# Performance work log

Measured on AMD Instinct MI355X. Metric: run time of the kernel, lower is better.

The kernel has to match this reference:

```python
import jax, jax.numpy as jnp
import numpy as np

B, T, H = 8, 8192, 512
E, R = 4, 16
SCALE = 0.04  # ~1/sqrt(H), keeps activations/logits in a sane range


def setup_inputs() -> dict:
    key = jax.random.key(0)
    ks = jax.random.split(key, 7)
    return {
        "x": jax.random.normal(ks[0], (B, T, H), jnp.float32),
        "gate_w": jax.random.normal(ks[1], (E, H), jnp.float32) * SCALE,
        "thr_w": jax.random.normal(ks[2], (1, H), jnp.float32) * SCALE,
        "fc1_w": jax.random.normal(ks[3], (E, H, H), jnp.float32) * SCALE,
        "lora_A": jax.random.normal(ks[4], (E, H, R), jnp.float32) * SCALE,
        "lora_B": jax.random.normal(ks[5], (E, R, H), jnp.float32) * SCALE,
        "fc2_w": jax.random.normal(ks[6], (E, H, H), jnp.float32) * SCALE,
    }


def reference(x, gate_w, thr_w, fc1_w, lora_A, lora_B, fc2_w):
    b, t, h = x.shape
    e = gate_w.shape[0]
    xf = x.reshape(-1, h)  # [N, H], N = B*T

    # Threshold-gated routing
    gate_logits = jax.nn.softmax(xf @ gate_w.T, axis=-1)          # [N, E]
    thresholds = jax.nn.sigmoid(xf @ thr_w.T) * (1.0 / e)         # [N, 1]
    adapted = gate_logits - thresholds                            # [N, E]
    selected = (adapted >= 0).astype(xf.dtype)                    # [N, E]
    weights = adapted * selected
    wsum = jnp.sum(weights, axis=-1, keepdims=True)
    wsum = jnp.where(wsum == 0, jnp.ones_like(wsum), wsum)
    weights = weights / wsum                                      # [N, E]

    # Experts: fc2(relu(fc1(x)) @ A @ B). Dense over all experts; the
    # weighted combine with zero weights matches the gather/scatter path.
    hidden = jax.nn.relu(jnp.einsum('ni,ehi->neh', xf, fc1_w))    # [N, E, H]
    lo = jnp.einsum('neh,ehr->ner', hidden, lora_A)               # [N, E, R]
    lo = jnp.einsum('ner,ero->neo', lo, lora_B)                   # [N, E, H]
    expert_out = jnp.einsum('neo,edo->ned', lo, fc2_w)            # [N, E, H]

    out = jnp.einsum('ne,ned->nd', weights, expert_out)           # [N, H]
    return out.reshape(b, t, h)
```

## Files before the change

kernel.cpp:

```cpp
#include <hip/hip_runtime.h>
#include <stdint.h>

#define NTOK 65536
#define HD   512
#define EXP  4
#define RK   16

typedef __attribute__((ext_vector_type(8)))  short short8;
typedef __attribute__((ext_vector_type(4)))  float f32x4;
typedef __attribute__((ext_vector_type(16))) float f32x16;

__device__ __forceinline__ unsigned short f2bf(float f) {
  union { float f; unsigned int u; } c; c.f = f;
  return (unsigned short)((c.u + 0x7fffu + ((c.u >> 16) & 1u)) >> 16);
}

__device__ __forceinline__ void gl_lds16(const void* g, void* l) {
  __builtin_amdgcn_global_load_lds((const __attribute__((address_space(1))) void*)g,
                                   (__attribute__((address_space(3))) void*)l, 16, 0, 0);
}

__global__ void convgate(const float* __restrict__ x, const float* __restrict__ gw,
                         const float* __restrict__ tw, unsigned short* __restrict__ xbo,
                         float* __restrict__ gates) {
  const int lane = threadIdx.x & 63;
  const int n = blockIdx.x * 4 + (threadIdx.x >> 6);
  const float4* xr = (const float4*)(x + (size_t)n * HD);
  const float4 xa = xr[lane * 2], xb = xr[lane * 2 + 1];
  ushort4 ua, ub;
  ua.x = f2bf(xa.x); ua.y = f2bf(xa.y); ua.z = f2bf(xa.z); ua.w = f2bf(xa.w);
  ub.x = f2bf(xb.x); ub.y = f2bf(xb.y); ub.z = f2bf(xb.z); ub.w = f2bf(xb.w);
  ushort4* xo = (ushort4*)(xbo + (size_t)n * HD);
  xo[lane * 2] = ua; xo[lane * 2 + 1] = ub;
  float s[5];
#pragma unroll
  for (int e = 0; e < 4; e++) {
    const float4* wr = (const float4*)(gw + e * HD);
    const float4 wa = wr[lane * 2], wb = wr[lane * 2 + 1];
    s[e] = xa.x * wa.x + xa.y * wa.y + xa.z * wa.z + xa.w * wa.w
         + xb.x * wb.x + xb.y * wb.y + xb.z * wb.z + xb.w * wb.w;
  }
  {
    const float4* wr = (const float4*)tw;
    const float4 wa = wr[lane * 2], wb = wr[lane * 2 + 1];
    s[4] = xa.x * wa.x + xa.y * wa.y + xa.z * wa.z + xa.w * wa.w
         + xb.x * wb.x + xb.y * wb.y + xb.z * wb.z + xb.w * wb.w;
  }
#pragma unroll
  for (int off = 32; off > 0; off >>= 1)
#pragma unroll
    for (int i = 0; i < 5; i++) s[i] += __shfl_xor(s[i], off, 64);
  float m = fmaxf(fmaxf(s[0], s[1]), fmaxf(s[2], s[3]));
  float e0 = expf(s[0] - m), e1 = expf(s[1] - m), e2 = expf(s[2] - m), e3 = expf(s[3] - m);
  float inv = 1.f / (e0 + e1 + e2 + e3);
  float thr = 0.25f / (1.f + expf(-s[4]));
  float a0 = e0 * inv - thr, a1 = e1 * inv - thr, a2 = e2 * inv - thr, a3 = e3 * inv - thr;
  float w0 = a0 > 0.f ? a0 : 0.f, w1 = a1 > 0.f ? a1 : 0.f;
  float w2 = a2 > 0.f ? a2 : 0.f, w3 = a3 > 0.f ? a3 : 0.f;
  float wsum = w0 + w1 + w2 + w3;
  wsum = (wsum == 0.f) ? 1.f : wsum;
  if (lane < 4) {
    float wv = lane == 0 ? w0 : lane == 1 ? w1 : lane == 2 ? w2 : w3;
    gates[(size_t)n * 4 + lane] = wv / wsum;
  }
}

__global__ void convk(const float* __restrict__ in, unsigned short* __restrict__ o, int n4) {
  int i = blockIdx.x * 256 + threadIdx.x;
  if (i < n4) {
    float4 v = ((const float4*)in)[i];
    ushort4 u;
    u.x = f2bf(v.x); u.y = f2bf(v.y); u.z = f2bf(v.z); u.w = f2bf(v.w);
    ((ushort4*)o)[i] = u;
  }
}

__global__ void prep_mt(const float* __restrict__ loraB, const float* __restrict__ fc2,
                        unsigned short* __restrict__ Mt) {
  int idx = blockIdx.x * 256 + threadIdx.x;
  int d  = idx & (HD - 1);
  int er = idx >> 9;
  int e = er >> 4, r = er & 15;
  const float4* B = (const float4*)(loraB + ((size_t)e * RK + r) * HD);
  const float4* F = (const float4*)(fc2 + ((size_t)e * HD + d) * HD);
  float a0 = 0.f, a1 = 0.f, a2 = 0.f, a3 = 0.f;
  for (int i = 0; i < HD / 4; i += 4) {
    float4 b0 = B[i],     f0 = F[i];
    float4 b1 = B[i + 1], f1 = F[i + 1];
    float4 b2 = B[i + 2], f2 = F[i + 2];
    float4 b3 = B[i + 3], f3 = F[i + 3];
    a0 += b0.x * f0.x + b0.y * f0.y + b0.z * f0.z + b0.w * f0.w;
    a1 += b1.x * f1.x + b1.y * f1.y + b1.z * f1.z + b1.w * f1.w;
    a2 += b2.x * f2.x + b2.y * f2.y + b2.z * f2.z + b2.w * f2.w;
    a3 += b3.x * f3.x + b3.y * f3.y + b3.z * f3.z + b3.w * f3.w;
  }
  Mt[d * 64 + er] = f2bf(a0 + a1 + a2 + a3);
}

__launch_bounds__(512, 2)
__global__ void fc1_lora(const unsigned short* __restrict__ xb,
                         const unsigned short* __restrict__ w1b,
                         const float* __restrict__ loraA,
                         float* __restrict__ lw) {
  __shared__ __align__(16) char smem[135168];
  const int bid = blockIdx.x;
  const int c = bid & 7;
  const int j = bid >> 3;
  const int eh = j & 7;
  const int e = eh >> 1, hq = eh & 1;
  const int ntile = c * 32 + (j >> 3);
  const int n0 = ntile * 256;
  const int tid = threadIdx.x;
  const int wave = tid >> 6, lane = tid & 63;
  const int l16 = lane & 15, quad = lane >> 4;
  const int l32 = lane & 31, half = lane >> 5;
  const int wr = wave >> 2, wc = wave & 3;

  const unsigned short* xg = xb + (size_t)n0 * HD;
  const unsigned short* wg = w1b + ((size_t)e * HD + (size_t)hq * 256) * HD;

  const unsigned short* xsrc[2];
  const unsigned short* wsrc[2];
#pragma unroll
  for (int i = 0; i < 2; i++) {
    const int sl = tid + 512 * i;
    const int sr = sl >> 3, g8 = (sl & 7) ^ (sr & 7);
    const int row = sr * 2 + (g8 >> 2), g = g8 & 3;
    xsrc[i] = xg + (size_t)row * HD + g * 8;
    wsrc[i] = wg + (size_t)row * HD + g * 8;
  }
  const int wbase = wave * 1024;

  int axo[2][4], bxo[2][2];
#pragma unroll
  for (int kk = 0; kk < 2; kk++) {
#pragma unroll
    for (int mb = 0; mb < 4; mb++) {
      const int rowa = wr * 128 + mb * 32 + l32;
      const int sr = rowa >> 1, g8 = (rowa & 1) * 4 + kk * 2 + half;
      axo[kk][mb] = (sr * 8 + (g8 ^ (sr & 7))) * 16;
    }
#pragma unroll
    for (int nb = 0; nb < 2; nb++) {
      const int rowb = wc * 64 + nb * 32 + l32;
      const int sr = rowb >> 1, g8 = (rowb & 1) * 4 + kk * 2 + half;
      bxo[kk][nb] = (sr * 8 + (g8 ^ (sr & 7))) * 16;
    }
  }

  f32x16 acc[4][2];
#pragma unroll
  for (int mb = 0; mb < 4; mb++)
#pragma unroll
    for (int nb = 0; nb < 2; nb++)
#pragma unroll
      for (int r = 0; r < 16; r++) acc[mb][nb][r] = 0.f;

#pragma unroll
  for (int tt = 0; tt < 3; tt++) {
    char* As = smem + tt * 32768;
#pragma unroll
    for (int i = 0; i < 2; i++) gl_lds16(xsrc[i] + tt * 32, As + wbase + 8192 * i);
#pragma unroll
    for (int i = 0; i < 2; i++) gl_lds16(wsrc[i] + tt * 32, As + 16384 + wbase + 8192 * i);
  }
  asm volatile("s_waitcnt vmcnt(8)\n\ts_barrier" ::: "memory");
  __builtin_amdgcn_sched_barrier(0);

#pragma unroll
  for (int t = 0; t < 16; t++) {
    char* Ab = smem + (t & 3) * 32768;
    char* Bb = Ab + 16384;
    char* As = smem + ((t + 3) & 3) * 32768;
    const int kos = (t + 3) * 32;
#pragma unroll
    for (int p = 0; p < 2; p++) {
      short8 af[4], bf[2];
#pragma unroll
      for (int mb = 0; mb < 4; mb++) af[mb] = *(const short8*)(Ab + axo[p][mb]);
#pragma unroll
      for (int nb = 0; nb < 2; nb++) bf[nb] = *(const short8*)(Bb + bxo[p][nb]);
      if (t < 13) {
        gl_lds16(xsrc[p] + kos, As + wbase + 8192 * p);
        gl_lds16(wsrc[p] + kos, As + 16384 + wbase + 8192 * p);
      }
      asm volatile("s_barrier" ::: "memory");
      __builtin_amdgcn_s_setprio(1);
#pragma unroll
      for (int mb = 0; mb < 4; mb++)
#pragma unroll
        for (int nb = 0; nb < 2; nb++)
          acc[mb][nb] = __builtin_amdgcn_mfma_f32_32x32x16_bf16(af[mb], bf[nb], acc[mb][nb], 0, 0, 0);
      __builtin_amdgcn_s_setprio(0);
    }
    if (t < 13) {
      asm volatile("s_waitcnt lgkmcnt(0)\n\ts_waitcnt vmcnt(8)\n\ts_barrier" ::: "memory");
    } else if (t == 13) {
      asm volatile("s_waitcnt lgkmcnt(0)\n\ts_waitcnt vmcnt(4)\n\ts_barrier" ::: "memory");
    } else if (t == 14) {
      asm volatile("s_waitcnt lgkmcnt(0)\n\ts_waitcnt vmcnt(0)\n\ts_barrier" ::: "memory");
    } else {
      asm volatile("s_waitcnt lgkmcnt(0)\n\ts_barrier" ::: "memory");
    }
    __builtin_amdgcn_sched_barrier(0);
  }

  unsigned short* hsm = (unsigned short*)smem;
#pragma unroll
  for (int mb = 0; mb < 4; mb++)
#pragma unroll
    for (int nb = 0; nb < 2; nb++) {
      const int colh = wc * 64 + nb * 32 + l32;
#pragma unroll
      for (int r = 0; r < 16; r++) {
        const int tok = wr * 128 + mb * 32 + 4 * half + (r & 3) + 8 * (r >> 2);
        float v = acc[mb][nb][r];
        v = v > 0.f ? v : 0.f;
        hsm[tok * 264 + colh] = f2bf(v);
      }
    }
  __syncthreads();

  const float* Ae = loraA + (size_t)e * HD * RK;
  const int hA0 = hq * 256;
  f32x4 lo[2];
#pragma unroll
  for (int mf = 0; mf < 2; mf++)
#pragma unroll
    for (int i = 0; i < 4; i++) lo[mf][i] = 0.f;
#pragma unroll
  for (int k2 = 0; k2 < 8; k2++) {
    short8 a2[2];
#pragma unroll
    for (int mf = 0; mf < 2; mf++) {
      const int tok = wave * 32 + mf * 16 + l16;
      a2[mf] = *(const short8*)(hsm + tok * 264 + k2 * 32 + quad * 8);
    }
    union { short8 v; unsigned short sv[8]; } b2;
#pragma unroll
    for (int j2 = 0; j2 < 8; j2++)
      b2.sv[j2] = f2bf(Ae[(size_t)(hA0 + k2 * 32 + quad * 8 + j2) * RK + l16]);
#pragma unroll
    for (int mf = 0; mf < 2; mf++)
      lo[mf] = __builtin_amdgcn_mfma_f32_16x16x32_bf16(a2[mf], b2.v, lo[mf], 0, 0, 0);
  }
#pragma unroll
  for (int mf = 0; mf < 2; mf++)
#pragma unroll
    for (int i = 0; i < 4; i++)
      atomicAdd(lw + (size_t)(n0 + wave * 32 + mf * 16 + quad * 4 + i) * 64 + e * 16 + l16, lo[mf][i]);
}

__launch_bounds__(256, 2)
__global__ void combine_k(const float* __restrict__ lw, const float* __restrict__ gates,
                          const unsigned short* __restrict__ Mt, float* __restrict__ out) {
  __shared__ __align__(16) char smem[65536];
  const int n0 = blockIdx.x * 64;
  const int tid = threadIdx.x;
  const int wave = tid >> 6, lane = tid & 63, quad = lane >> 4, l16 = lane & 15;
#pragma unroll
  for (int i = 0; i < 16; i++) {
    const int slot = tid + 256 * i;
    const int row = slot >> 3;
    const int g = (slot & 7) ^ (row & 7);
    *(uint4*)(smem + slot * 16) = *(const uint4*)(Mt + row * 64 + g * 8);
  }
  __syncthreads();
  f32x4 acc[4][8];
#pragma unroll
  for (int a = 0; a < 4; a++)
#pragma unroll
    for (int b = 0; b < 8; b++)
#pragma unroll
      for (int i = 0; i < 4; i++) acc[a][b][i] = 0.f;
#pragma unroll
  for (int ks = 0; ks < 2; ks++) {
    short8 af[4], bfr[8];
#pragma unroll
    for (int mf = 0; mf < 4; mf++) {
      const int n = n0 + mf * 16 + l16;
      const float* lr = lw + (size_t)n * 64 + ks * 32 + quad * 8;
      float4 u0 = *(const float4*)lr;
      float4 u1 = *(const float4*)(lr + 4);
      const float g = gates[(size_t)n * 4 + ((ks * 32 + quad * 8) >> 4)];
      union { short8 v; unsigned short s[8]; } a;
      a.s[0] = f2bf(u0.x * g); a.s[1] = f2bf(u0.y * g);
      a.s[2] = f2bf(u0.z * g); a.s[3] = f2bf(u0.w * g);
      a.s[4] = f2bf(u1.x * g); a.s[5] = f2bf(u1.y * g);
      a.s[6] = f2bf(u1.z * g); a.s[7] = f2bf(u1.w * g);
      af[mf] = a.v;
    }
#pragma unroll
    for (int nf = 0; nf < 8; nf++) {
      const int row = wave * 128 + nf * 16 + l16;
      const int slot = row * 8 + ((ks * 4 + quad) ^ (row & 7));
      bfr[nf] = *(const short8*)(smem + slot * 16);
    }
#pragma unroll
    for (int mf = 0; mf < 4; mf++)
#pragma unroll
      for (int nf = 0; nf < 8; nf++)
        acc[mf][nf] = __builtin_amdgcn_mfma_f32_16x16x32_bf16(af[mf], bfr[nf], acc[mf][nf], 0, 0, 0);
  }
#pragma unroll
  for (int mf = 0; mf < 4; mf++)
#pragma unroll
    for (int nf = 0; nf < 8; nf++) {
      const int d = wave * 128 + nf * 16 + l16;
#pragma unroll
      for (int i = 0; i < 4; i++)
        out[(size_t)(n0 + mf * 16 + quad * 4 + i) * HD + d] = acc[mf][nf][i];
    }
}

extern "C" void kernel_launch(void* const* d_in, const int* in_sizes, int n_in,
                              void* d_out, int out_size, void* d_ws, size_t ws_size,
                              hipStream_t stream) {
  const float* x      = (const float*)d_in[0];
  const float* gate_w = (const float*)d_in[1];
  const float* thr_w  = (const float*)d_in[2];
  const float* fc1_w  = (const float*)d_in[3];
  const float* lora_A = (const float*)d_in[4];
  const float* lora_B = (const float*)d_in[5];
  const float* fc2_w  = (const float*)d_in[6];
  float* out = (float*)d_out;
  char* ws = (char*)d_ws;

  unsigned short* xbp = (unsigned short*)(ws);
  unsigned short* w1b = (unsigned short*)(ws + 67108864);
  unsigned short* Mt  = (unsigned short*)(ws + 69206016);
  float*          gts = (float*)(ws + 69271552);
  float*          lwp = (float*)(ws + 70320128);

  hipMemsetAsync(lwp, 0, (size_t)NTOK * 64 * sizeof(float), stream);
  convgate<<<NTOK / 4, 256, 0, stream>>>(x, gate_w, thr_w, xbp, gts);
  convk<<<1024, 256, 0, stream>>>(fc1_w, w1b, EXP * HD * HD / 4);
  prep_mt<<<128, 256, 0, stream>>>(lora_B, fc2_w, Mt);
  fc1_lora<<<2048, 512, 0, stream>>>(xbp, w1b, lora_A, lwp);
  combine_k<<<NTOK / 64, 256, 0, stream>>>(lwp, gts, Mt, out);
}
```

Baseline: 440.7 us.

## Parallelize prep_mt per wave, pre-transpose lora_A, coalesce combine stores, retune barriers

Result: no change. 441.4 us (+0.2%).

```diff
diff --git a/kernel.cpp b/kernel.cpp
--- a/kernel.cpp
+++ b/kernel.cpp
@@ -77,30 +77,34 @@
 
 __global__ void prep_mt(const float* __restrict__ loraB, const float* __restrict__ fc2,
                         unsigned short* __restrict__ Mt) {
+  const int wid = blockIdx.x * 4 + (threadIdx.x >> 6);
+  const int lane = threadIdx.x & 63;
+  const int d = wid & (HD - 1);
+  const int er = wid >> 9;
+  const int e = er >> 4, r = er & 15;
+  const float4* B = (const float4*)(loraB + ((size_t)e * RK + r) * HD);
+  const float4* F = (const float4*)(fc2 + ((size_t)e * HD + d) * HD);
+  const float4 b0 = B[lane * 2], b1 = B[lane * 2 + 1];
+  const float4 f0 = F[lane * 2], f1 = F[lane * 2 + 1];
+  float s = b0.x * f0.x + b0.y * f0.y + b0.z * f0.z + b0.w * f0.w
+          + b1.x * f1.x + b1.y * f1.y + b1.z * f1.z + b1.w * f1.w;
+#pragma unroll
+  for (int off = 32; off > 0; off >>= 1) s += __shfl_xor(s, off, 64);
+  if (lane == 0) Mt[d * 64 + er] = f2bf(s);
+}
+
+__global__ void prep_la(const float* __restrict__ la, unsigned short* __restrict__ laT) {
   int idx = blockIdx.x * 256 + threadIdx.x;
-  int d  = idx & (HD - 1);
+  int h = idx & (HD - 1);
   int er = idx >> 9;
   int e = er >> 4, r = er & 15;
-  const float4* B = (const float4*)(loraB + ((size_t)e * RK + r) * HD);
-  const float4* F = (const float4*)(fc2 + ((size_t)e * HD + d) * HD);
-  float a0 = 0.f, a1 = 0.f, a2 = 0.f, a3 = 0.f;
-  for (int i = 0; i < HD / 4; i += 4) {
-    float4 b0 = B[i],     f0 = F[i];
-    float4 b1 = B[i + 1], f1 = F[i + 1];
-    float4 b2 = B[i + 2], f2 = F[i + 2];
-    float4 b3 = B[i + 3], f3 = F[i + 3];
-    a0 += b0.x * f0.x + b0.y * f0.y + b0.z * f0.z + b0.w * f0.w;
-    a1 += b1.x * f1.x + b1.y * f1.y + b1.z * f1.z + b1.w * f1.w;
-    a2 += b2.x * f2.x + b2.y * f2.y + b2.z * f2.z + b2.w * f2.w;
-    a3 += b3.x * f3.x + b3.y * f3.y + b3.z * f3.z + b3.w * f3.w;
-  }
-  Mt[d * 64 + er] = f2bf(a0 + a1 + a2 + a3);
+  laT[(size_t)er * HD + h] = f2bf(la[((size_t)e * HD + h) * RK + r]);
 }
 
 __launch_bounds__(512, 2)
 __global__ void fc1_lora(const unsigned short* __restrict__ xb,
                          const unsigned short* __restrict__ w1b,
-                         const float* __restrict__ loraA,
+                         const unsigned short* __restrict__ laT,
                          float* __restrict__ lw) {
   __shared__ __align__(16) char smem[135168];
   const int bid = blockIdx.x;
@@ -133,18 +137,18 @@
 
   int axo[2][4], bxo[2][2];
 #pragma unroll
-  for (int kk = 0; kk < 2; kk++) {
+  for (int p = 0; p < 2; p++) {
 #pragma unroll
     for (int mb = 0; mb < 4; mb++) {
       const int rowa = wr * 128 + mb * 32 + l32;
-      const int sr = rowa >> 1, g8 = (rowa & 1) * 4 + kk * 2 + half;
-      axo[kk][mb] = (sr * 8 + (g8 ^ (sr & 7))) * 16;
+      const int sr = rowa >> 1, g8 = (rowa & 1) * 4 + p * 2 + half;
+      axo[p][mb] = (sr * 8 + (g8 ^ (sr & 7))) * 16;
     }
 #pragma unroll
     for (int nb = 0; nb < 2; nb++) {
       const int rowb = wc * 64 + nb * 32 + l32;
-      const int sr = rowb >> 1, g8 = (rowb & 1) * 4 + kk * 2 + half;
-      bxo[kk][nb] = (sr * 8 + (g8 ^ (sr & 7))) * 16;
+      const int sr = rowb >> 1, g8 = (rowb & 1) * 4 + p * 2 + half;
+      bxo[p][nb] = (sr * 8 + (g8 ^ (sr & 7))) * 16;
     }
   }
 
@@ -164,7 +168,8 @@
 #pragma unroll
     for (int i = 0; i < 2; i++) gl_lds16(wsrc[i] + tt * 32, As + 16384 + wbase + 8192 * i);
   }
-  asm volatile("s_waitcnt vmcnt(8)\n\ts_barrier" ::: "memory");
+  asm volatile("s_waitcnt vmcnt(8)" ::: "memory");
+  __builtin_amdgcn_s_barrier();
   __builtin_amdgcn_sched_barrier(0);
 
 #pragma unroll
@@ -184,7 +189,9 @@
         gl_lds16(xsrc[p] + kos, As + wbase + 8192 * p);
         gl_lds16(wsrc[p] + kos, As + 16384 + wbase + 8192 * p);
       }
-      asm volatile("s_barrier" ::: "memory");
+      __builtin_amdgcn_s_barrier();
+      asm volatile("s_waitcnt lgkmcnt(0)" ::: "memory");
+      __builtin_amdgcn_sched_barrier(0);
       __builtin_amdgcn_s_setprio(1);
 #pragma unroll
       for (int mb = 0; mb < 4; mb++)
@@ -192,17 +199,16 @@
         for (int nb = 0; nb < 2; nb++)
           acc[mb][nb] = __builtin_amdgcn_mfma_f32_32x32x16_bf16(af[mb], bf[nb], acc[mb][nb], 0, 0, 0);
       __builtin_amdgcn_s_setprio(0);
-    }
-    if (t < 13) {
-      asm volatile("s_waitcnt lgkmcnt(0)\n\ts_waitcnt vmcnt(8)\n\ts_barrier" ::: "memory");
-    } else if (t == 13) {
-      asm volatile("s_waitcnt lgkmcnt(0)\n\ts_waitcnt vmcnt(4)\n\ts_barrier" ::: "memory");
-    } else if (t == 14) {
-      asm volatile("s_waitcnt lgkmcnt(0)\n\ts_waitcnt vmcnt(0)\n\ts_barrier" ::: "memory");
-    } else {
-      asm volatile("s_waitcnt lgkmcnt(0)\n\ts_barrier" ::: "memory");
-    }
-    __builtin_amdgcn_sched_barrier(0);
+      if (p == 0) {
+        __builtin_amdgcn_s_barrier();
+      } else {
+        if (t < 13)       asm volatile("s_waitcnt vmcnt(8)" ::: "memory");
+        else if (t == 13) asm volatile("s_waitcnt vmcnt(4)" ::: "memory");
+        else if (t == 14) asm volatile("s_waitcnt vmcnt(0)" ::: "memory");
+        __builtin_amdgcn_s_barrier();
+      }
+      __builtin_amdgcn_sched_barrier(0);
+    }
   }
 
   unsigned short* hsm = (unsigned short*)smem;
@@ -221,8 +227,7 @@
     }
   __syncthreads();
 
-  const float* Ae = loraA + (size_t)e * HD * RK;
-  const int hA0 = hq * 256;
+  const unsigned short* laTe = laT + (size_t)(e * 16 + l16) * HD + hq * 256;
   f32x4 lo[2];
 #pragma unroll
   for (int mf = 0; mf < 2; mf++)
@@ -230,19 +235,13 @@
     for (int i = 0; i < 4; i++) lo[mf][i] = 0.f;
 #pragma unroll
   for (int k2 = 0; k2 < 8; k2++) {
-    short8 a2[2];
+    const short8 b2 = *(const short8*)(laTe + k2 * 32 + quad * 8);
 #pragma unroll
     for (int mf = 0; mf < 2; mf++) {
       const int tok = wave * 32 + mf * 16 + l16;
-      a2[mf] = *(const short8*)(hsm + tok * 264 + k2 * 32 + quad * 8);
-    }
-    union { short8 v; unsigned short sv[8]; } b2;
-#pragma unroll
-    for (int j2 = 0; j2 < 8; j2++)
-      b2.sv[j2] = f2bf(Ae[(size_t)(hA0 + k2 * 32 + quad * 8 + j2) * RK + l16]);
-#pragma unroll
-    for (int mf = 0; mf < 2; mf++)
-      lo[mf] = __builtin_amdgcn_mfma_f32_16x16x32_bf16(a2[mf], b2.v, lo[mf], 0, 0, 0);
+      const short8 a2 = *(const short8*)(hsm + tok * 264 + k2 * 32 + quad * 8);
+      lo[mf] = __builtin_amdgcn_mfma_f32_16x16x32_bf16(a2, b2, lo[mf], 0, 0, 0);
+    }
   }
 #pragma unroll
   for (int mf = 0; mf < 2; mf++)
@@ -302,14 +301,16 @@
       for (int nf = 0; nf < 8; nf++)
         acc[mf][nf] = __builtin_amdgcn_mfma_f32_16x16x32_bf16(af[mf], bfr[nf], acc[mf][nf], 0, 0, 0);
   }
+  __syncthreads();
+  float* scr = (float*)smem + wave * 320;
 #pragma unroll
   for (int mf = 0; mf < 4; mf++)
 #pragma unroll
     for (int nf = 0; nf < 8; nf++) {
-      const int d = wave * 128 + nf * 16 + l16;
-#pragma unroll
-      for (int i = 0; i < 4; i++)
-        out[(size_t)(n0 + mf * 16 + quad * 4 + i) * HD + d] = acc[mf][nf][i];
+#pragma unroll
+      for (int i = 0; i < 4; i++) scr[(quad * 4 + i) * 20 + l16] = acc[mf][nf][i];
+      float4 v = *(const float4*)(scr + l16 * 20 + quad * 4);
+      *(float4*)(out + (size_t)(n0 + mf * 16 + l16) * HD + wave * 128 + nf * 16 + quad * 4) = v;
     }
 }
 
@@ -331,11 +332,13 @@
   unsigned short* Mt  = (unsigned short*)(ws + 69206016);
   float*          gts = (float*)(ws + 69271552);
   float*          lwp = (float*)(ws + 70320128);
+  unsigned short* laT = (unsigned short*)(ws + 87097344);
 
   hipMemsetAsync(lwp, 0, (size_t)NTOK * 64 * sizeof(float), stream);
   convgate<<<NTOK / 4, 256, 0, stream>>>(x, gate_w, thr_w, xbp, gts);
   convk<<<1024, 256, 0, stream>>>(fc1_w, w1b, EXP * HD * HD / 4);
-  prep_mt<<<128, 256, 0, stream>>>(lora_B, fc2_w, Mt);
-  fc1_lora<<<2048, 512, 0, stream>>>(xbp, w1b, lora_A, lwp);
+  prep_mt<<<8192, 256, 0, stream>>>(lora_B, fc2_w, Mt);
+  prep_la<<<128, 256, 0, stream>>>(lora_A, laT);
+  fc1_lora<<<2048, 512, 0, stream>>>(xbp, w1b, laT, lwp);
   combine_k<<<NTOK / 64, 256, 0, stream>>>(lwp, gts, Mt, out);
 }
```
